# Kernel tuning notes

Hardware: AMD Instinct MI355X
Metric: run time of the kernel (lower is better)

## Reference

```python
import jax, jax.numpy as jnp
import numpy as np

H = 768        # bert hidden_size
HID = 512      # lstm_hidden
HALF = HID // 2
T = 20         # tagset_size
START, STOP = 18, 19
S = 16386      # input positions incl. CLS/SEP
NEG = -10000.0


def setup_inputs() -> dict:
    key = jax.random.key(0)
    ks = jax.random.split(key, 12)
    sc_x = 1.0
    x = jax.random.normal(ks[0], (1, S, H), dtype=jnp.float32)
    # PyTorch LSTM params (gate order i,f,g,o), one layer, bidirectional
    s_ih = 1.0 / np.sqrt(HALF)
    w_ih_f = jax.random.uniform(ks[1], (4 * HALF, H), jnp.float32, -s_ih, s_ih)
    w_hh_f = jax.random.uniform(ks[2], (4 * HALF, HALF), jnp.float32, -s_ih, s_ih)
    b_ih_f = jax.random.uniform(ks[3], (4 * HALF,), jnp.float32, -s_ih, s_ih)
    b_hh_f = jax.random.uniform(ks[4], (4 * HALF,), jnp.float32, -s_ih, s_ih)
    w_ih_b = jax.random.uniform(ks[5], (4 * HALF, H), jnp.float32, -s_ih, s_ih)
    w_hh_b = jax.random.uniform(ks[6], (4 * HALF, HALF), jnp.float32, -s_ih, s_ih)
    b_ih_b = jax.random.uniform(ks[7], (4 * HALF,), jnp.float32, -s_ih, s_ih)
    b_hh_b = jax.random.uniform(ks[8], (4 * HALF,), jnp.float32, -s_ih, s_ih)
    s_t = 1.0 / np.sqrt(HID)
    w_tag = jax.random.uniform(ks[9], (T, HID), jnp.float32, -s_t, s_t)
    b_tag = jax.random.uniform(ks[10], (T,), jnp.float32, -s_t, s_t)
    transitions = jax.random.normal(ks[11], (T, T), dtype=jnp.float32)
    transitions = transitions.at[START, :].set(NEG).at[:, STOP].set(NEG)
    return {
        "x": x,
        "w_ih_f": w_ih_f, "w_hh_f": w_hh_f, "b_ih_f": b_ih_f, "b_hh_f": b_hh_f,
        "w_ih_b": w_ih_b, "w_hh_b": w_hh_b, "b_ih_b": b_ih_b, "b_hh_b": b_hh_b,
        "w_tag": w_tag, "b_tag": b_tag, "transitions": transitions,
    }


def _lstm_one_step(xt, w_ih, b_ih, b_hh):
    # Original passes [1, N, H] to a batch_first=False LSTM => seq_len=1,
    # batch=N, zero initial state. So each token does ONE cell step:
    # h0=c0=0 => hh contribution is only b_hh.
    g = xt @ w_ih.T + b_ih + b_hh          # [N, 4*HALF]
    i, f, gg, o = jnp.split(g, 4, axis=-1)  # PyTorch gate order i,f,g,o
    c = jax.nn.sigmoid(i) * jnp.tanh(gg)    # f*c0 = 0
    return jax.nn.sigmoid(o) * jnp.tanh(c)  # [N, HALF]


def reference(x, w_ih_f, w_hh_f, b_ih_f, b_hh_f,
              w_ih_b, w_hh_b, b_ih_b, b_hh_b,
              w_tag, b_tag, transitions):
    tok = x[0, 1:-1, :]                     # narrow(1,1,S-2): drop CLS/SEP -> [N,H]
    h_f = _lstm_one_step(tok, w_ih_f, b_ih_f, b_hh_f)
    h_b = _lstm_one_step(tok, w_ih_b, b_ih_b, b_hh_b)
    enc = jnp.concatenate([h_f, h_b], axis=-1)   # [N, HID]
    feats = enc @ w_tag.T + b_tag                # [N, T] emission scores

    # ---- Viterbi decode (sequential DP over tokens) ----
    init = jnp.full((T,), NEG, dtype=feats.dtype).at[START].set(0.0)

    def vstep(fv, feat):
        scores = fv[None, :] + transitions       # [next_tag, prev_tag]
        bp = jnp.argmax(scores, axis=1)          # backpointers [T]
        fv_new = jnp.max(scores, axis=1) + feat
        return fv_new, bp

    fv, bps = jax.lax.scan(vstep, init, feats)   # bps: [N, T]
    terminal = fv + transitions[STOP]
    best = jnp.argmax(terminal)
    path_score = terminal[best]

    def btrack(b, bp):
        return bp[b], b                          # emit tag at time t, move to t-1

    _, best_path = jax.lax.scan(btrack, best, bps, reverse=True)  # [N] in time order
    return path_score, best_path
```

## Files before the change

kernel.cpp:

```cpp
#include <hip/hip_runtime.h>
#include <math.h>

#define HDIM 768
#define HIDD 512
#define NTOK 16384
#define NT 20
#define CHUNKS 128
#define CLEN 128

typedef unsigned short ushort_t;
typedef __attribute__((ext_vector_type(8))) short bf16x8;
typedef __attribute__((ext_vector_type(4))) float f32x4;

__device__ __forceinline__ float sigm(float x){ return 1.0f/(1.0f+expf(-x)); }

__device__ __forceinline__ ushort_t f2bf(float f){
    unsigned int u = __float_as_uint(f);
    unsigned int r = (u + 0x7fffu + ((u >> 16) & 1u)) >> 16;
    return (ushort_t)r;
}
__device__ __forceinline__ float bf2f(ushort_t b){
    return __uint_as_float(((unsigned int)b) << 16);
}

#define GLD16(gp, lp) __builtin_amdgcn_global_load_lds( \
    (const __attribute__((address_space(1))) void*)(gp), \
    (__attribute__((address_space(3))) void*)(lp), 16, 0, 0)

__global__ __launch_bounds__(256) void conv_kernel(
    const float* __restrict__ x,
    const float* __restrict__ wf, const float* __restrict__ wb,
    ushort_t* __restrict__ Ah, ushort_t* __restrict__ Al,
    ushort_t* __restrict__ Bh, ushort_t* __restrict__ Bl)
{
    const int bid = blockIdx.x;
    if (bid < 1152){
        int t = bid*256 + threadIdx.x;
        int n = t / 192, c4 = (t - n*192)*4;
        int dir = n / 768, nr = n - dir*768;
        int gate = nr >> 8, j = nr & 255;
        int wrow = j + ((gate==0)?0:((gate==1)?512:768));
        const float* src = dir ? wb : wf;
        const float4 v = *(const float4*)(src + (size_t)wrow*HDIM + c4);
        float f[4] = {v.x, v.y, v.z, v.w};
        ushort_t h[4], l[4];
        #pragma unroll
        for (int i=0;i<4;++i){
            h[i] = f2bf(f[i]);
            l[i] = f2bf(f[i] - bf2f(h[i]));
        }
        *(ushort4*)(Bh + (size_t)n*HDIM + c4) = make_ushort4(h[0],h[1],h[2],h[3]);
        *(ushort4*)(Bl + (size_t)n*HDIM + c4) = make_ushort4(l[0],l[1],l[2],l[3]);
    } else {
        int t = (bid-1152)*256 + threadIdx.x;
        int row = t / 192, c4 = (t - row*192)*4;
        const float4 v = *(const float4*)(x + (size_t)(row+1)*HDIM + c4);
        float f[4] = {v.x, v.y, v.z, v.w};
        ushort_t h[4], l[4];
        #pragma unroll
        for (int i=0;i<4;++i){
            h[i] = f2bf(f[i]);
            l[i] = f2bf(f[i] - bf2f(h[i]));
        }
        *(ushort4*)(Ah + (size_t)row*HDIM + c4) = make_ushort4(h[0],h[1],h[2],h[3]);
        *(ushort4*)(Al + (size_t)row*HDIM + c4) = make_ushort4(l[0],l[1],l[2],l[3]);
    }
}

__global__ __launch_bounds__(256, 2) void gemm_fused(
    const ushort_t* __restrict__ Ah, const ushort_t* __restrict__ Al,
    const ushort_t* __restrict__ Bh, const ushort_t* __restrict__ Bl,
    const float* __restrict__ bihf, const float* __restrict__ bhhf,
    const float* __restrict__ bihb, const float* __restrict__ bhhb,
    const float* __restrict__ wtag, float* __restrict__ featsp)
{
    __shared__ __align__(16) char smem[81920];
    float* hbuf = (float*)smem;
    float* wts  = (float*)(smem + 16640);

    const int tid = threadIdx.x;
    const int bx = blockIdx.x;
    const int xcd = bx & 7, g3 = bx >> 3;
    const int q = g3 & 7, mt = (g3 >> 3)*8 + xcd;
    const int dir = q >> 2, j0 = (q & 3)*64;
    const int row0 = mt*128;
    const float* __restrict__ bih = dir ? bihb : bihf;
    const float* __restrict__ bhh = dir ? bhhb : bhhf;

    const int lane = tid & 63, wv = tid >> 6;
    const int wm = wv >> 1, wn = wv & 1;
    const int lm = lane & 15, lq = lane >> 4;
    const int wbB = (tid & 192) * 16;

    const int P_ = tid >> 3, s_ = tid & 7;
    const int q_ = s_ ^ (P_ & 7);
    const int mA = (P_ << 1) | (q_ >> 2);
    const int k8s = q_ & 3;
    const size_t aoff0 = (size_t)(row0 + mA)*HDIM + k8s*8;
    const size_t aoff1 = (size_t)(row0 + 64 + mA)*HDIM + k8s*8;
    size_t bOff[3];
    #pragma unroll
    for (int g=0; g<3; ++g)
        bOff[g] = (size_t)(dir*768 + g*256 + j0 + mA)*HDIM + k8s*8;

    int aoffB[4], boffB[2];
    #pragma unroll
    for (int f=0; f<4; ++f){
        int m = wm*64 + f*16 + lm;
        int rg = m >> 6, r = m & 63;
        aoffB[f] = rg*4096 + ((r>>1)*8 + ((((r&1)<<2)|lq) ^ ((r>>1)&7)))*16;
    }
    #pragma unroll
    for (int f=0; f<2; ++f){
        int n = wn*32 + f*16 + lm;
        boffB[f] = ((n>>1)*8 + ((((n&1)<<2)|lq) ^ ((n>>1)&7)))*16;
    }

    int jcol[2];
    #pragma unroll
    for (int f=0; f<2; ++f) jcol[f] = j0 + wn*32 + f*16 + lm;

    f32x4 acc[3][4][2];
    #pragma unroll
    for (int g=0; g<3; ++g)
        #pragma unroll
        for (int fm=0; fm<4; ++fm)
            #pragma unroll
            for (int fn=0; fn<2; ++fn)
                acc[g][fm][fn] = (f32x4){0.f,0.f,0.f,0.f};

    {
        GLD16(Ah + aoff0, smem + wbB);
        GLD16(Ah + aoff1, smem + 4096 + wbB);
        GLD16(Al + aoff0, smem + 8192 + wbB);
        GLD16(Al + aoff1, smem + 12288 + wbB);
        char* bb = smem + 32768;
        #pragma unroll
        for (int g=0; g<3; ++g){
            GLD16(Bh + bOff[g], bb + g*8192 + wbB);
            GLD16(Bl + bOff[g], bb + g*8192 + 4096 + wbB);
        }
    }

    #pragma unroll 1
    for (int kt=0; kt<24; ++kt){
        __syncthreads();

        if (kt < 23){
            const int k0n = (kt+1)*32;
            char* ab = smem + ((kt+1)&1)*16384;
            char* bb = smem + 32768 + ((kt+1)&1)*24576;
            GLD16(Ah + aoff0 + k0n, ab + wbB);
            GLD16(Ah + aoff1 + k0n, ab + 4096 + wbB);
            GLD16(Al + aoff0 + k0n, ab + 8192 + wbB);
            GLD16(Al + aoff1 + k0n, ab + 12288 + wbB);
            #pragma unroll
            for (int g=0; g<3; ++g){
                GLD16(Bh + bOff[g] + k0n, bb + g*8192 + wbB);
                GLD16(Bl + bOff[g] + k0n, bb + g*8192 + 4096 + wbB);
            }
        }

        const char* ab = smem + (kt&1)*16384;
        const char* bb = smem + 32768 + (kt&1)*24576;
        bf16x8 afh[4], afl[4];
        #pragma unroll
        for (int f=0; f<4; ++f){
            afh[f] = *(const bf16x8*)(ab + aoffB[f]);
            afl[f] = *(const bf16x8*)(ab + 8192 + aoffB[f]);
        }
        #pragma unroll
        for (int g=0; g<3; ++g){
            const char* bg = bb + g*8192;
            #pragma unroll
            for (int fn=0; fn<2; ++fn){
                bf16x8 bh = *(const bf16x8*)(bg + boffB[fn]);
                bf16x8 bl = *(const bf16x8*)(bg + 4096 + boffB[fn]);
                #pragma unroll
                for (int fm=0; fm<4; ++fm){
                    acc[g][fm][fn] = __builtin_amdgcn_mfma_f32_16x16x32_bf16(
                        afh[fm], bh, acc[g][fm][fn], 0, 0, 0);
                    acc[g][fm][fn] = __builtin_amdgcn_mfma_f32_16x16x32_bf16(
                        afl[fm], bh, acc[g][fm][fn], 0, 0, 0);
                    acc[g][fm][fn] = __builtin_amdgcn_mfma_f32_16x16x32_bf16(
                        afh[fm], bl, acc[g][fm][fn], 0, 0, 0);
                }
            }
        }
    }

    float bi[2], bg_[2], bo[2];
    #pragma unroll
    for (int f=0; f<2; ++f){
        bi[f]  = bih[jcol[f]]       + bhh[jcol[f]];
        bg_[f] = bih[512 + jcol[f]] + bhh[512 + jcol[f]];
        bo[f]  = bih[768 + jcol[f]] + bhh[768 + jcol[f]];
    }
    float hv[4][2][4];
    #pragma unroll
    for (int fm=0; fm<4; ++fm)
        #pragma unroll
        for (int fn=0; fn<2; ++fn)
            #pragma unroll
            for (int r=0; r<4; ++r){
                float cv = sigm(acc[0][fm][fn][r] + bi[fn]) *
                           tanhf(acc[1][fm][fn][r] + bg_[fn]);
                hv[fm][fn][r] = sigm(acc[2][fm][fn][r] + bo[fn]) * tanhf(cv);
            }

    __syncthreads();
    for (int i2=tid; i2<NT*64; i2+=256){
        int t = i2 >> 6, j = i2 & 63;
        wts[i2] = wtag[t*HIDD + dir*256 + j0 + j];
    }
    float* fq = featsp + (size_t)q * (NTOK*NT);
    #pragma unroll 1
    for (int ph=0; ph<2; ++ph){
        __syncthreads();
        if (wm == ph){
            #pragma unroll
            for (int fm=0; fm<4; ++fm)
                #pragma unroll
                for (int fn=0; fn<2; ++fn)
                    #pragma unroll
                    for (int r=0; r<4; ++r){
                        int mloc = fm*16 + lq*4 + r;
                        int jloc = wn*32 + fn*16 + lm;
                        hbuf[mloc*65 + jloc] = hv[fm][fn][r];
                    }
        }
        __syncthreads();
        const int mrow = tid & 63, grp = tid >> 6;
        const int tg0 = grp*5;
        float s[5] = {0.f,0.f,0.f,0.f,0.f};
        for (int j=0;j<64;++j){
            float h = hbuf[mrow*65 + j];
            #pragma unroll
            for (int tt=0; tt<5; ++tt)
                s[tt] = fmaf(h, wts[(tg0+tt)*64 + j], s[tt]);
        }
        const int mglob = row0 + ph*64 + mrow;
        #pragma unroll
        for (int tt=0; tt<5; ++tt)
            fq[(size_t)mglob*NT + tg0 + tt] = s[tt];
    }
}

__device__ __forceinline__ void load_fl(
    const float* __restrict__ featsp, const float* __restrict__ btg,
    float* fl, int c, int tid, int nthr)
{
    const int base = c*(CLEN*NT/4);
    for (int idx=tid; idx<CLEN*NT/4; idx+=nthr){
        float4 s[8];
        #pragma unroll
        for (int p=0; p<8; ++p)
            s[p] = ((const float4*)(featsp + (size_t)p*NTOK*NT))[base+idx];
        float4 v;
        v.x = ((s[0].x+s[1].x)+(s[2].x+s[3].x)) + ((s[4].x+s[5].x)+(s[6].x+s[7].x));
        v.y = ((s[0].y+s[1].y)+(s[2].y+s[3].y)) + ((s[4].y+s[5].y)+(s[6].y+s[7].y));
        v.z = ((s[0].z+s[1].z)+(s[2].z+s[3].z)) + ((s[4].z+s[5].z)+(s[6].z+s[7].z));
        v.w = ((s[0].w+s[1].w)+(s[2].w+s[3].w)) + ((s[4].w+s[5].w)+(s[6].w+s[7].w));
        int t0 = (idx*4) % 20;
        v.x += btg[t0]; v.y += btg[t0+1]; v.z += btg[t0+2]; v.w += btg[t0+3];
        ((float4*)fl)[idx] = v;
    }
}

__global__ __launch_bounds__(512) void vit_chunkmat(
    const float* __restrict__ featsp, const float* __restrict__ btag,
    const float* __restrict__ trans, float* __restrict__ Pall)
{
    __shared__ float fl[CLEN*NT];
    __shared__ float Pb[2][NT*NT];
    const int c = blockIdx.x, tid = threadIdx.x;
    load_fl(featsp, btag, fl, c, tid, 512);
    const bool act = tid < NT*NT;
    const int i = tid/20, j = tid - i*20;
    float tr[NT];
    if (act){
        #pragma unroll
        for (int k=0;k<NT;++k) tr[k] = trans[i*NT+k];
        Pb[0][tid] = (i==j) ? 0.f : -1e30f;
    }
    __syncthreads();
    int cur = 0;
    for (int t=0;t<CLEN;++t){
        float m = -3.0e38f;
        if (act){
            #pragma unroll
            for (int k=0;k<NT;++k) m = fmaxf(m, tr[k] + Pb[cur][k*NT+j]);
            m += fl[t*NT+i];
            Pb[cur^1][tid] = m;
        }
        __syncthreads();
        cur ^= 1;
    }
    if (act) Pall[(size_t)c*(NT*NT) + tid] = Pb[cur][tid];
}

__global__ __launch_bounds__(128) void vit_scan(
    const float* __restrict__ Pall, const float* __restrict__ trans,
    float* __restrict__ fvstart, float* __restrict__ dout, int* __restrict__ bestws)
{
    __shared__ float Pb[NT*NT];
    __shared__ float fv[NT];
    const int tid = threadIdx.x;
    float4 pn = {0.f,0.f,0.f,0.f};
    if (tid<100) pn = ((const float4*)Pall)[tid];
    if (tid<NT) fv[tid] = (tid==18) ? 0.f : -10000.f;
    for (int c=0;c<CHUNKS;++c){
        if (tid<100) ((float4*)Pb)[tid] = pn;
        if (tid<100 && c+1<CHUNKS) pn = ((const float4*)(Pall + (size_t)(c+1)*(NT*NT)))[tid];
        __syncthreads();
        if (tid<NT) fvstart[c*NT+tid] = fv[tid];
        float nf = -3.0e38f;
        if (tid<NT){
            #pragma unroll
            for (int j=0;j<NT;++j) nf = fmaxf(nf, Pb[tid*NT+j] + fv[j]);
        }
        __syncthreads();
        if (tid<NT) fv[tid] = nf;
    }
    __syncthreads();
    if (tid==0){
        float best = -3.0e38f; int bidx = 0;
        for (int j=0;j<NT;++j){
            float tv = fv[j] + trans[19*NT+j];
            if (tv > best){ best = tv; bidx = j; }
        }
        dout[0] = best;
        bestws[0] = bidx;
    }
}

__global__ __launch_bounds__(128) void vit_replay(
    const float* __restrict__ featsp, const float* __restrict__ btag,
    const float* __restrict__ trans, const float* __restrict__ fvstart,
    unsigned int* __restrict__ bpout, int* __restrict__ Hout)
{
    __shared__ float fl[CLEN*NT];
    __shared__ float fv[NT];
    __shared__ unsigned char bp[CLEN*NT];
    const int c = blockIdx.x, tid = threadIdx.x;
    load_fl(featsp, btag, fl, c, tid, 128);
    float tr[NT];
    if (tid<NT){
        fv[tid] = fvstart[c*NT+tid];
        #pragma unroll
        for (int k=0;k<NT;++k) tr[k] = trans[tid*NT+k];
    }
    __syncthreads();
    for (int t=0;t<CLEN;++t){
        float best = 0.f; int bj = 0;
        if (tid<NT){
            best = tr[0] + fv[0];
            #pragma unroll
            for (int j=1;j<NT;++j){
                float v = tr[j] + fv[j];
                if (v > best){ best = v; bj = j; }
            }
        }
        __syncthreads();
        if (tid<NT){
            fv[tid] = best + fl[t*NT+tid];
            bp[t*NT+tid] = (unsigned char)bj;
        }
        __syncthreads();
    }
    for (int idx=tid; idx<CLEN*NT/4; idx+=128)
        bpout[(size_t)c*(CLEN*NT/4) + idx] = ((unsigned int*)bp)[idx];
    if (tid<NT){
        int m = tid;
        for (int t=CLEN-1;t>=0;--t) m = bp[t*NT+m];
        Hout[c*NT+tid] = m;
    }
}

__global__ __launch_bounds__(64) void bt_fill(
    const unsigned int* __restrict__ bpin, const int* __restrict__ Hin,
    const int* __restrict__ bestws, float* __restrict__ dout)
{
    __shared__ int Hl[CHUNKS*NT];
    __shared__ unsigned char bp[CLEN*NT];
    __shared__ float ob[CLEN];
    const int c = blockIdx.x, tid = threadIdx.x;
    for (int idx=tid; idx<CHUNKS*NT; idx+=64) Hl[idx] = Hin[idx];
    for (int idx=tid; idx<CLEN*NT/4; idx+=64)
        ((unsigned int*)bp)[idx] = bpin[(size_t)c*(CLEN*NT/4) + idx];
    __syncthreads();
    if (tid==0){
        int e = bestws[0];
        for (int cc=CHUNKS-1; cc>c; --cc) e = Hl[cc*NT+e];
        for (int t=CLEN-1;t>=0;--t){ ob[t] = (float)e; e = bp[t*NT+e]; }
    }
    __syncthreads();
    for (int idx=tid; idx<CLEN; idx+=64)
        dout[1 + c*CLEN + idx] = ob[idx];
}

extern "C" void kernel_launch(void* const* d_in, const int* in_sizes, int n_in,
                              void* d_out, int out_size, void* d_ws, size_t ws_size,
                              hipStream_t stream)
{
    const float* x    = (const float*)d_in[0];
    const float* wf   = (const float*)d_in[1];
    const float* bihf = (const float*)d_in[3];
    const float* bhhf = (const float*)d_in[4];
    const float* wb   = (const float*)d_in[5];
    const float* bihb = (const float*)d_in[7];
    const float* bhhb = (const float*)d_in[8];
    const float* wtag = (const float*)d_in[9];
    const float* btag = (const float*)d_in[10];
    const float* trans= (const float*)d_in[11];
    float* out = (float*)d_out;

    char* w = (char*)d_ws;
    ushort_t* Ah = (ushort_t*)w;         w += 25165824;
    ushort_t* Al = (ushort_t*)w;         w += 25165824;
    ushort_t* Bh = (ushort_t*)w;         w += 2359296;
    ushort_t* Bl = (ushort_t*)w;         w += 2359296;
    float* featsp = (float*)w;           w += 10485760;
    float* Pall  = (float*)w;            w += 204800;
    float* fvst  = (float*)w;            w += 10240;
    int* Hmap    = (int*)w;              w += 10240;
    unsigned int* bp = (unsigned int*)w; w += 327680;
    int* best    = (int*)w;

    conv_kernel<<<13440, 256, 0, stream>>>(x, wf, wb, Ah, Al, Bh, Bl);
    gemm_fused<<<1024, 256, 0, stream>>>(Ah, Al, Bh, Bl, bihf, bhhf, bihb, bhhb,
                                         wtag, featsp);
    vit_chunkmat<<<CHUNKS, 512, 0, stream>>>(featsp, btag, trans, Pall);
    vit_scan<<<1, 128, 0, stream>>>(Pall, trans, fvst, out, best);
    vit_replay<<<CHUNKS, 128, 0, stream>>>(featsp, btag, trans, fvst, bp, Hmap);
    bt_fill<<<CHUNKS, 64, 0, stream>>>(bp, Hmap, best, out);
}
```

Before: 372.4 us.

## Split GEMM k-loop into per-gate phases with fine-grained vmcnt waits and setprio

```diff
diff --git a/kernel.cpp b/kernel.cpp
--- a/kernel.cpp
+++ b/kernel.cpp
@@ -67,6 +67,35 @@
     }
 }
 
+#define VMCNT(n) asm volatile("s_waitcnt vmcnt(" #n ")" ::: "memory")
+#define LGKM0()  do{ asm volatile("s_waitcnt lgkmcnt(0)" ::: "memory"); \
+                     __builtin_amdgcn_sched_barrier(0); }while(0)
+
+#define MFMA_CLUSTER(g, BH0, BL0, BH1, BL1) do{                               \
+    _Pragma("unroll")                                                         \
+    for (int fm=0; fm<4; ++fm){                                               \
+        acc[g][fm][0] = __builtin_amdgcn_mfma_f32_16x16x32_bf16(afh[fm], BH0, \
+                            acc[g][fm][0], 0, 0, 0);                          \
+        acc[g][fm][0] = __builtin_amdgcn_mfma_f32_16x16x32_bf16(afl[fm], BH0, \
+                            acc[g][fm][0], 0, 0, 0);                          \
+        acc[g][fm][0] = __builtin_amdgcn_mfma_f32_16x16x32_bf16(afh[fm], BL0, \
+                            acc[g][fm][0], 0, 0, 0);                          \
+    }                                                                         \
+    _Pragma("unroll")                                                         \
+    for (int fm=0; fm<4; ++fm){                                               \
+        acc[g][fm][1] = __builtin_amdgcn_mfma_f32_16x16x32_bf16(afh[fm], BH1, \
+                            acc[g][fm][1], 0, 0, 0);                          \
+        acc[g][fm][1] = __builtin_amdgcn_mfma_f32_16x16x32_bf16(afl[fm], BH1, \
+                            acc[g][fm][1], 0, 0, 0);                          \
+        acc[g][fm][1] = __builtin_amdgcn_mfma_f32_16x16x32_bf16(afh[fm], BL1, \
+                            acc[g][fm][1], 0, 0, 0);                          \
+    }                                                                         \
+}while(0)
+
+#define READ_A(ab) do{ _Pragma("unroll") for (int f=0; f<4; ++f){             \
+    afh[f] = *(const bf16x8*)((ab) + aoffB[f]);                               \
+    afl[f] = *(const bf16x8*)((ab) + 8192 + aoffB[f]); } }while(0)
+
 __global__ __launch_bounds__(256, 2) void gemm_fused(
     const ushort_t* __restrict__ Ah, const ushort_t* __restrict__ Al,
     const ushort_t* __restrict__ Bh, const ushort_t* __restrict__ Bl,
@@ -129,63 +158,130 @@
             for (int fn=0; fn<2; ++fn)
                 acc[g][fm][fn] = (f32x4){0.f,0.f,0.f,0.f};
 
+    bf16x8 afh[4], afl[4];
+
     {
-        GLD16(Ah + aoff0, smem + wbB);
-        GLD16(Ah + aoff1, smem + 4096 + wbB);
-        GLD16(Al + aoff0, smem + 8192 + wbB);
-        GLD16(Al + aoff1, smem + 12288 + wbB);
+        char* ab = smem;
         char* bb = smem + 32768;
-        #pragma unroll
-        for (int g=0; g<3; ++g){
-            GLD16(Bh + bOff[g], bb + g*8192 + wbB);
-            GLD16(Bl + bOff[g], bb + g*8192 + 4096 + wbB);
-        }
+        GLD16(Ah + aoff0, ab + wbB);
+        GLD16(Ah + aoff1, ab + 4096 + wbB);
+        GLD16(Al + aoff0, ab + 8192 + wbB);
+        GLD16(Al + aoff1, ab + 12288 + wbB);
+        GLD16(Bh + bOff[0], bb + wbB);
+        GLD16(Bl + bOff[0], bb + 4096 + wbB);
+        GLD16(Bh + bOff[1], bb + 8192 + wbB);
+        GLD16(Bl + bOff[1], bb + 12288 + wbB);
+        GLD16(Bh + bOff[2], bb + 16384 + wbB);
+        GLD16(Bl + bOff[2], bb + 20480 + wbB);
     }
 
     #pragma unroll 1
-    for (int kt=0; kt<24; ++kt){
-        __syncthreads();
-
-        if (kt < 23){
-            const int k0n = (kt+1)*32;
-            char* ab = smem + ((kt+1)&1)*16384;
-            char* bb = smem + 32768 + ((kt+1)&1)*24576;
-            GLD16(Ah + aoff0 + k0n, ab + wbB);
-            GLD16(Ah + aoff1 + k0n, ab + 4096 + wbB);
-            GLD16(Al + aoff0 + k0n, ab + 8192 + wbB);
-            GLD16(Al + aoff1 + k0n, ab + 12288 + wbB);
-            #pragma unroll
-            for (int g=0; g<3; ++g){
-                GLD16(Bh + bOff[g] + k0n, bb + g*8192 + wbB);
-                GLD16(Bl + bOff[g] + k0n, bb + g*8192 + 4096 + wbB);
-            }
-        }
-
+    for (int kt=0; kt<23; ++kt){
         const char* ab = smem + (kt&1)*16384;
         const char* bb = smem + 32768 + (kt&1)*24576;
-        bf16x8 afh[4], afl[4];
-        #pragma unroll
-        for (int f=0; f<4; ++f){
-            afh[f] = *(const bf16x8*)(ab + aoffB[f]);
-            afl[f] = *(const bf16x8*)(ab + 8192 + aoffB[f]);
-        }
-        #pragma unroll
-        for (int g=0; g<3; ++g){
-            const char* bg = bb + g*8192;
-            #pragma unroll
-            for (int fn=0; fn<2; ++fn){
-                bf16x8 bh = *(const bf16x8*)(bg + boffB[fn]);
-                bf16x8 bl = *(const bf16x8*)(bg + 4096 + boffB[fn]);
-                #pragma unroll
-                for (int fm=0; fm<4; ++fm){
-                    acc[g][fm][fn] = __builtin_amdgcn_mfma_f32_16x16x32_bf16(
-                        afh[fm], bh, acc[g][fm][fn], 0, 0, 0);
-                    acc[g][fm][fn] = __builtin_amdgcn_mfma_f32_16x16x32_bf16(
-                        afl[fm], bh, acc[g][fm][fn], 0, 0, 0);
-                    acc[g][fm][fn] = __builtin_amdgcn_mfma_f32_16x16x32_bf16(
-                        afh[fm], bl, acc[g][fm][fn], 0, 0, 0);
-                }
-            }
+        char* abn = smem + ((kt+1)&1)*16384;
+        char* bbn = smem + 32768 + ((kt+1)&1)*24576;
+        const int k0n = (kt+1)*32;
+
+        VMCNT(4);
+        __builtin_amdgcn_s_barrier();
+        READ_A(ab);
+        {
+            bf16x8 bh0 = *(const bf16x8*)(bb + boffB[0]);
+            bf16x8 bl0 = *(const bf16x8*)(bb + 4096 + boffB[0]);
+            bf16x8 bh1 = *(const bf16x8*)(bb + boffB[1]);
+            bf16x8 bl1 = *(const bf16x8*)(bb + 4096 + boffB[1]);
+            GLD16(Ah + aoff0 + k0n, abn + wbB);
+            GLD16(Ah + aoff1 + k0n, abn + 4096 + wbB);
+            GLD16(Al + aoff0 + k0n, abn + 8192 + wbB);
+            GLD16(Al + aoff1 + k0n, abn + 12288 + wbB);
+            GLD16(Bh + bOff[0] + k0n, bbn + wbB);
+            GLD16(Bl + bOff[0] + k0n, bbn + 4096 + wbB);
+            LGKM0();
+            __builtin_amdgcn_s_setprio(1);
+            MFMA_CLUSTER(0, bh0, bl0, bh1, bl1);
+            __builtin_amdgcn_s_setprio(0);
+            __builtin_amdgcn_sched_barrier(0);
+        }
+
+        VMCNT(8);
+        __builtin_amdgcn_s_barrier();
+        {
+            bf16x8 bh0 = *(const bf16x8*)(bb + 8192 + boffB[0]);
+            bf16x8 bl0 = *(const bf16x8*)(bb + 12288 + boffB[0]);
+            bf16x8 bh1 = *(const bf16x8*)(bb + 8192 + boffB[1]);
+            bf16x8 bl1 = *(const bf16x8*)(bb + 12288 + boffB[1]);
+            GLD16(Bh + bOff[1] + k0n, bbn + 8192 + wbB);
+            GLD16(Bl + bOff[1] + k0n, bbn + 12288 + wbB);
+            LGKM0();
+            __builtin_amdgcn_s_setprio(1);
+            MFMA_CLUSTER(1, bh0, bl0, bh1, bl1);
+            __builtin_amdgcn_s_setprio(0);
+            __builtin_amdgcn_sched_barrier(0);
+        }
+
+        VMCNT(8);
+        __builtin_amdgcn_s_barrier();
+        {
+            bf16x8 bh0 = *(const bf16x8*)(bb + 16384 + boffB[0]);
+            bf16x8 bl0 = *(const bf16x8*)(bb + 20480 + boffB[0]);
+            bf16x8 bh1 = *(const bf16x8*)(bb + 16384 + boffB[1]);
+            bf16x8 bl1 = *(const bf16x8*)(bb + 20480 + boffB[1]);
+            GLD16(Bh + bOff[2] + k0n, bbn + 16384 + wbB);
+            GLD16(Bl + bOff[2] + k0n, bbn + 20480 + wbB);
+            LGKM0();
+            __builtin_amdgcn_s_setprio(1);
+            MFMA_CLUSTER(2, bh0, bl0, bh1, bl1);
+            __builtin_amdgcn_s_setprio(0);
+            __builtin_amdgcn_sched_barrier(0);
+        }
+    }
+
+    {
+        const char* ab = smem + 16384;
+        const char* bb = smem + 32768 + 24576;
+
+        VMCNT(4);
+        __builtin_amdgcn_s_barrier();
+        READ_A(ab);
+        {
+            bf16x8 bh0 = *(const bf16x8*)(bb + boffB[0]);
+            bf16x8 bl0 = *(const bf16x8*)(bb + 4096 + boffB[0]);
+            bf16x8 bh1 = *(const bf16x8*)(bb + boffB[1]);
+            bf16x8 bl1 = *(const bf16x8*)(bb + 4096 + boffB[1]);
+            LGKM0();
+            __builtin_amdgcn_s_setprio(1);
+            MFMA_CLUSTER(0, bh0, bl0, bh1, bl1);
+            __builtin_amdgcn_s_setprio(0);
+            __builtin_amdgcn_sched_barrier(0);
+        }
+
+        VMCNT(2);
+        __builtin_amdgcn_s_barrier();
+        {
+            bf16x8 bh0 = *(const bf16x8*)(bb + 8192 + boffB[0]);
+            bf16x8 bl0 = *(const bf16x8*)(bb + 12288 + boffB[0]);
+            bf16x8 bh1 = *(const bf16x8*)(bb + 8192 + boffB[1]);
+            bf16x8 bl1 = *(const bf16x8*)(bb + 12288 + boffB[1]);
+            LGKM0();
+            __builtin_amdgcn_s_setprio(1);
+            MFMA_CLUSTER(1, bh0, bl0, bh1, bl1);
+            __builtin_amdgcn_s_setprio(0);
+            __builtin_amdgcn_sched_barrier(0);
+        }
+
+        VMCNT(0);
+        __builtin_amdgcn_s_barrier();
+        {
+            bf16x8 bh0 = *(const bf16x8*)(bb + 16384 + boffB[0]);
+            bf16x8 bl0 = *(const bf16x8*)(bb + 20480 + boffB[0]);
+            bf16x8 bh1 = *(const bf16x8*)(bb + 16384 + boffB[1]);
+            bf16x8 bl1 = *(const bf16x8*)(bb + 20480 + boffB[1]);
+            LGKM0();
+            __builtin_amdgcn_s_setprio(1);
+            MFMA_CLUSTER(2, bh0, bl0, bh1, bl1);
+            __builtin_amdgcn_s_setprio(0);
+            __builtin_amdgcn_sched_barrier(0);
         }
     }
 
```

New measurement: 366.4 us. No clear change (-1.6%).

## Software-pipeline GEMM k-loop with per-gate staged loads, vmcnt waits and MFMA priority

Applied to the files above, without the earlier changes.

```diff
diff --git a/kernel.cpp b/kernel.cpp
--- a/kernel.cpp
+++ b/kernel.cpp
@@ -67,6 +67,67 @@
     }
 }
 
+#define VMCNT(n) asm volatile("s_waitcnt vmcnt(" #n ")" ::: "memory")
+#define BARRIER() asm volatile("s_barrier" ::: "memory")
+
+#define READ_BG(g, bb) do{                                                    \
+    bfr[g][0] = *(const bf16x8*)((bb) + (g)*8192 + boffB[0]);                 \
+    bfr[g][1] = *(const bf16x8*)((bb) + (g)*8192 + 4096 + boffB[0]);          \
+    bfr[g][2] = *(const bf16x8*)((bb) + (g)*8192 + boffB[1]);                 \
+    bfr[g][3] = *(const bf16x8*)((bb) + (g)*8192 + 4096 + boffB[1]);          \
+}while(0)
+
+#define READ_A(S, ab) do{ _Pragma("unroll") for (int f=0; f<4; ++f){          \
+    aH##S[f] = *(const bf16x8*)((ab) + aoffB[f]);                             \
+    aL##S[f] = *(const bf16x8*)((ab) + 8192 + aoffB[f]); } }while(0)
+
+#define MFMA_CLUSTER(g, S) do{                                                \
+  __builtin_amdgcn_s_setprio(1);                                              \
+  _Pragma("unroll")                                                           \
+  for (int fn=0; fn<2; ++fn){                                                 \
+    _Pragma("unroll")                                                         \
+    for (int fm=0; fm<4; ++fm){                                               \
+      acc[g][fm][fn] = __builtin_amdgcn_mfma_f32_16x16x32_bf16(aH##S[fm],     \
+          bfr[g][fn*2], acc[g][fm][fn], 0, 0, 0);                             \
+      acc[g][fm][fn] = __builtin_amdgcn_mfma_f32_16x16x32_bf16(aL##S[fm],     \
+          bfr[g][fn*2], acc[g][fm][fn], 0, 0, 0);                             \
+      acc[g][fm][fn] = __builtin_amdgcn_mfma_f32_16x16x32_bf16(aH##S[fm],     \
+          bfr[g][fn*2+1], acc[g][fm][fn], 0, 0, 0);                           \
+    }                                                                         \
+  }                                                                           \
+  __builtin_amdgcn_s_setprio(0);                                              \
+}while(0)
+
+#define KT_BODY(kt, P, CUR, NXT) do{                                          \
+    const int k0n = ((kt)+1)*32;                                              \
+    char* abn = smem + (1-(P))*16384;                                         \
+    char* bbn = smem + 32768 + (1-(P))*24576;                                 \
+    const char* bbc = smem + 32768 + (P)*24576;                               \
+                  \
+    GLD16(Ah + aoff0 + k0n, abn + wbB);                                       \
+    GLD16(Ah + aoff1 + k0n, abn + 4096 + wbB);                                \
+    GLD16(Al + aoff0 + k0n, abn + 8192 + wbB);                                \
+    GLD16(Al + aoff1 + k0n, abn + 12288 + wbB);                               \
+    GLD16(Bh + bOff[0] + k0n, bbn + wbB);                                     \
+    GLD16(Bl + bOff[0] + k0n, bbn + 4096 + wbB);                              \
+    VMCNT(8); BARRIER();                                                      \
+    READ_BG(1, bbc);                                                          \
+    MFMA_CLUSTER(0, CUR);                                                     \
+                  \
+    GLD16(Bh + bOff[1] + k0n, bbn + 8192 + wbB);                              \
+    GLD16(Bl + bOff[1] + k0n, bbn + 12288 + wbB);                             \
+    VMCNT(8); BARRIER();                                                      \
+    READ_BG(2, bbc);                                                          \
+    MFMA_CLUSTER(1, CUR);                                                     \
+              \
+    GLD16(Bh + bOff[2] + k0n, bbn + 16384 + wbB);                             \
+    GLD16(Bl + bOff[2] + k0n, bbn + 20480 + wbB);                             \
+    VMCNT(4); BARRIER();                                                      \
+    READ_A(NXT, abn);                                                         \
+    READ_BG(0, bbn);                                                          \
+    MFMA_CLUSTER(2, CUR);                                                     \
+}while(0)
+
 __global__ __launch_bounds__(256, 2) void gemm_fused(
     const ushort_t* __restrict__ Ah, const ushort_t* __restrict__ Al,
     const ushort_t* __restrict__ Bh, const ushort_t* __restrict__ Bl,
@@ -116,10 +177,6 @@
         boffB[f] = ((n>>1)*8 + ((((n&1)<<2)|lq) ^ ((n>>1)&7)))*16;
     }
 
-    int jcol[2];
-    #pragma unroll
-    for (int f=0; f<2; ++f) jcol[f] = j0 + wn*32 + f*16 + lm;
-
     f32x4 acc[3][4][2];
     #pragma unroll
     for (int g=0; g<3; ++g)
@@ -129,65 +186,49 @@
             for (int fn=0; fn<2; ++fn)
                 acc[g][fm][fn] = (f32x4){0.f,0.f,0.f,0.f};
 
+    bf16x8 aH0[4], aL0[4], aH1[4], aL1[4];
+    bf16x8 bfr[3][4];
+
     {
-        GLD16(Ah + aoff0, smem + wbB);
-        GLD16(Ah + aoff1, smem + 4096 + wbB);
-        GLD16(Al + aoff0, smem + 8192 + wbB);
-        GLD16(Al + aoff1, smem + 12288 + wbB);
+        char* ab = smem;
         char* bb = smem + 32768;
-        #pragma unroll
-        for (int g=0; g<3; ++g){
-            GLD16(Bh + bOff[g], bb + g*8192 + wbB);
-            GLD16(Bl + bOff[g], bb + g*8192 + 4096 + wbB);
-        }
+        GLD16(Ah + aoff0, ab + wbB);
+        GLD16(Ah + aoff1, ab + 4096 + wbB);
+        GLD16(Al + aoff0, ab + 8192 + wbB);
+        GLD16(Al + aoff1, ab + 12288 + wbB);
+        GLD16(Bh + bOff[0], bb + wbB);
+        GLD16(Bl + bOff[0], bb + 4096 + wbB);
+        GLD16(Bh + bOff[1], bb + 8192 + wbB);
+        GLD16(Bl + bOff[1], bb + 12288 + wbB);
+        GLD16(Bh + bOff[2], bb + 16384 + wbB);
+        GLD16(Bl + bOff[2], bb + 20480 + wbB);
+        VMCNT(4); BARRIER();
+        READ_A(0, (const char*)smem);
+        READ_BG(0, (const char*)(smem + 32768));
     }
 
     #pragma unroll 1
-    for (int kt=0; kt<24; ++kt){
-        __syncthreads();
-
-        if (kt < 23){
-            const int k0n = (kt+1)*32;
-            char* ab = smem + ((kt+1)&1)*16384;
-            char* bb = smem + 32768 + ((kt+1)&1)*24576;
-            GLD16(Ah + aoff0 + k0n, ab + wbB);
-            GLD16(Ah + aoff1 + k0n, ab + 4096 + wbB);
-            GLD16(Al + aoff0 + k0n, ab + 8192 + wbB);
-            GLD16(Al + aoff1 + k0n, ab + 12288 + wbB);
-            #pragma unroll
-            for (int g=0; g<3; ++g){
-                GLD16(Bh + bOff[g] + k0n, bb + g*8192 + wbB);
-                GLD16(Bl + bOff[g] + k0n, bb + g*8192 + 4096 + wbB);
-            }
-        }
-
-        const char* ab = smem + (kt&1)*16384;
-        const char* bb = smem + 32768 + (kt&1)*24576;
-        bf16x8 afh[4], afl[4];
-        #pragma unroll
-        for (int f=0; f<4; ++f){
-            afh[f] = *(const bf16x8*)(ab + aoffB[f]);
-            afl[f] = *(const bf16x8*)(ab + 8192 + aoffB[f]);
-        }
-        #pragma unroll
-        for (int g=0; g<3; ++g){
-            const char* bg = bb + g*8192;
-            #pragma unroll
-            for (int fn=0; fn<2; ++fn){
-                bf16x8 bh = *(const bf16x8*)(bg + boffB[fn]);
-                bf16x8 bl = *(const bf16x8*)(bg + 4096 + boffB[fn]);
-                #pragma unroll
-                for (int fm=0; fm<4; ++fm){
-                    acc[g][fm][fn] = __builtin_amdgcn_mfma_f32_16x16x32_bf16(
-                        afh[fm], bh, acc[g][fm][fn], 0, 0, 0);
-                    acc[g][fm][fn] = __builtin_amdgcn_mfma_f32_16x16x32_bf16(
-                        afl[fm], bh, acc[g][fm][fn], 0, 0, 0);
-                    acc[g][fm][fn] = __builtin_amdgcn_mfma_f32_16x16x32_bf16(
-                        afh[fm], bl, acc[g][fm][fn], 0, 0, 0);
-                }
-            }
-        }
-    }
+    for (int kt2 = 0; kt2 < 11; ++kt2){
+        const int kt = kt2*2;
+        KT_BODY(kt,   0, 0, 1);
+        KT_BODY(kt+1, 1, 1, 0);
+    }
+    KT_BODY(22, 0, 0, 1);
+
+    {
+        const char* bbc = smem + 32768 + 24576;
+        VMCNT(2); BARRIER();
+        READ_BG(1, bbc);
+        MFMA_CLUSTER(0, 1);
+        VMCNT(0); BARRIER();
+        READ_BG(2, bbc);
+        MFMA_CLUSTER(1, 1);
+        MFMA_CLUSTER(2, 1);
+    }
+
+    int jcol[2];
+    #pragma unroll
+    for (int f=0; f<2; ++f) jcol[f] = j0 + wn*32 + f*16 + lm;
 
     float bi[2], bg_[2], bo[2];
     #pragma unroll
```

Measured after the change: 372.3 us. About the same (-0.0%).
